# Optimization experiments

Measured on AMD Instinct MI355X. Metric: run time of the kernel, lower is better.

## Reference

```python
import jax, jax.numpy as jnp
import numpy as np

BN_EPS = 1e-5
N_NODES = 100000
N_EDGES = 1600000
IN_DIM = 128
HID = 256   # 2 * out_dim
OUT_DIM = 128


def setup_inputs() -> dict:
    key = jax.random.key(0)
    ks = jax.random.split(key, 8)
    x = jax.random.normal(ks[0], (N_NODES, IN_DIM), dtype=jnp.float32)
    edge_index = jax.random.randint(ks[1], (2, N_EDGES), 0, N_NODES, dtype=jnp.int32)
    # GINConv learned eps (train_eps=True), init 0
    eps = jnp.zeros((), dtype=jnp.float32)
    # MLP: Linear(in, 2*out) -> BN -> ReLU -> Linear(2*out, out)
    s1 = 1.0 / np.sqrt(IN_DIM)
    s2 = 1.0 / np.sqrt(HID)
    W1 = jax.random.uniform(ks[2], (IN_DIM, HID), jnp.float32, -s1, s1)
    b1 = jax.random.uniform(ks[3], (HID,), jnp.float32, -s1, s1)
    g1 = jnp.ones((HID,), jnp.float32)
    beta1 = jnp.zeros((HID,), jnp.float32)
    W2 = jax.random.uniform(ks[4], (HID, OUT_DIM), jnp.float32, -s2, s2)
    b2 = jax.random.uniform(ks[5], (OUT_DIM,), jnp.float32, -s2, s2)
    # outer BatchNorm
    g2 = jnp.ones((OUT_DIM,), jnp.float32)
    beta2 = jnp.zeros((OUT_DIM,), jnp.float32)
    return {"x": x, "edge_index": edge_index, "eps": eps,
            "W1": W1, "b1": b1, "g1": g1, "beta1": beta1,
            "W2": W2, "b2": b2, "g2": g2, "beta2": beta2}


def _batchnorm(h, gamma, beta):
    # training-mode BatchNorm1d: batch mean, biased variance
    mu = jnp.mean(h, axis=0)
    var = jnp.mean(jnp.square(h - mu), axis=0)
    return (h - mu) * jax.lax.rsqrt(var + BN_EPS) * gamma + beta


def reference(x, edge_index, eps, W1, b1, g1, beta1, W2, b2, g2, beta2):
    src, dst = edge_index[0], edge_index[1]
    # sum-aggregation of neighbor features: scatter-add x[src] onto dst
    aggr = jax.ops.segment_sum(x[src], dst, num_segments=x.shape[0])  # [N, in_dim]
    h = (1.0 + eps) * x + aggr
    # MLP: Linear -> BN -> ReLU -> Linear
    h = h @ W1 + b1
    h = jax.nn.relu(_batchnorm(h, g1, beta1))
    h = h @ W2 + b2
    # outer BN + ReLU
    return jax.nn.relu(_batchnorm(h, g2, beta2))
```

## Files before the change

### kernel.cpp

```cpp
#include <hip/hip_runtime.h>
#include <hip/hip_bf16.h>

#define N_NODES 100000
#define N_EDGES 1600000
#define IN_DIM  128
#define HID     256
#define OUT_DIM 128
#define BN_EPS  1e-5f

typedef unsigned int u32;
typedef unsigned short u16;
typedef __attribute__((ext_vector_type(8))) short short8v;
typedef __attribute__((ext_vector_type(4))) float f32x4;

__device__ __forceinline__ float bf2f(u16 h) {
    return __uint_as_float(((u32)h) << 16);
}
__device__ __forceinline__ u16 f2bf(float f) {
    u32 u = __float_as_uint(f);
    u32 r = (u + 0x7fffu + ((u >> 16) & 1u)) >> 16;
    return (u16)r;
}
__device__ __forceinline__ u32 pack2(float a, float b) {
    return (u32)f2bf(a) | ((u32)f2bf(b) << 16);
}
__device__ __forceinline__ void gload16(const void* g, void* l) {
    __builtin_amdgcn_global_load_lds((const __attribute__((address_space(1))) u32*)g,
                                     (__attribute__((address_space(3))) u32*)l, 16, 0, 0);
}
#define MFMA(a,b,c) __builtin_amdgcn_mfma_f32_16x16x32_bf16(a, b, c, 0, 0, 0)

__global__ __launch_bounds__(256) void k_prep(const float* __restrict__ x,
                                              const int* __restrict__ ei,
                                              const float* __restrict__ W1,
                                              const float* __restrict__ W2,
                                              uint2* __restrict__ xb,
                                              int* __restrict__ head2,
                                              int2* __restrict__ nxt,
                                              char* __restrict__ w1t,
                                              char* __restrict__ w2t) {
    int t = blockIdx.x * 256 + threadIdx.x;
    {
        float4 v = ((const float4*)x)[t];
        uint2 p;
        p.x = pack2(v.x, v.y);
        p.y = pack2(v.z, v.w);
        xb[t] = p;
    }
    if (t < N_EDGES) {
        int dst = ei[N_EDGES + t];
        int src = ei[t];
        int old = atomicExch(&head2[dst * 2 + (t & 1)], t);
        nxt[t] = make_int2(old, src);
    }
    if (t < 8192) {
        u16 tmp[8];
        if (t < 4096) {
            int j = t >> 4, kc = t & 15;
            #pragma unroll
            for (int i = 0; i < 8; ++i) tmp[i] = f2bf(W1[(kc * 8 + i) * HID + j]);
            u32 off = ((u32)(j * 256 + kc * 16)) ^ (((u32)(j & 7)) << 4);
            uint4 q;
            q.x = (u32)tmp[0] | ((u32)tmp[1] << 16);
            q.y = (u32)tmp[2] | ((u32)tmp[3] << 16);
            q.z = (u32)tmp[4] | ((u32)tmp[5] << 16);
            q.w = (u32)tmp[6] | ((u32)tmp[7] << 16);
            *(uint4*)(w1t + off) = q;
        } else {
            int t2 = t - 4096;
            int j = t2 >> 5, kc = t2 & 31;
            #pragma unroll
            for (int i = 0; i < 8; ++i) tmp[i] = f2bf(W2[(kc * 8 + i) * OUT_DIM + j]);
            u32 off = ((u32)(j * 512 + kc * 16)) ^ (((u32)(j & 7)) << 4);
            uint4 q;
            q.x = (u32)tmp[0] | ((u32)tmp[1] << 16);
            q.y = (u32)tmp[2] | ((u32)tmp[3] << 16);
            q.z = (u32)tmp[4] | ((u32)tmp[5] << 16);
            q.w = (u32)tmp[6] | ((u32)tmp[7] << 16);
            *(uint4*)(w2t + off) = q;
        }
    }
}

__global__ __launch_bounds__(256) void k_aggregate(const uint4* __restrict__ xb4,
                                                   const int2* __restrict__ nxt,
                                                   const int* __restrict__ head2,
                                                   const float* __restrict__ epsp,
                                                   char* __restrict__ aggrb) {
    const int lane = threadIdx.x & 63;
    const int w = threadIdx.x >> 6;
    const int q = lane >> 4, l = lane & 15;
    const int nq = q >> 1, p = q & 1;
    const int node = blockIdx.x * 8 + w * 2 + nq;

    float a[8];
    #pragma unroll
    for (int i = 0; i < 8; ++i) a[i] = 0.f;

    if (p == 0) {
        float sc = 1.0f + epsp[0];
        uint4 v = xb4[node * 16 + l];
        a[0] = bf2f((u16)v.x) * sc;  a[1] = bf2f((u16)(v.x >> 16)) * sc;
        a[2] = bf2f((u16)v.y) * sc;  a[3] = bf2f((u16)(v.y >> 16)) * sc;
        a[4] = bf2f((u16)v.z) * sc;  a[5] = bf2f((u16)(v.z >> 16)) * sc;
        a[6] = bf2f((u16)v.w) * sc;  a[7] = bf2f((u16)(v.w >> 16)) * sc;
    }
    int e = head2[node * 2 + p];
    while (e >= 0) {
        int2 nv = nxt[e];
        e = nv.x;
        uint4 v = xb4[nv.y * 16 + l];
        a[0] += bf2f((u16)v.x);  a[1] += bf2f((u16)(v.x >> 16));
        a[2] += bf2f((u16)v.y);  a[3] += bf2f((u16)(v.y >> 16));
        a[4] += bf2f((u16)v.z);  a[5] += bf2f((u16)(v.z >> 16));
        a[6] += bf2f((u16)v.w);  a[7] += bf2f((u16)(v.w >> 16));
    }
    #pragma unroll
    for (int i = 0; i < 8; ++i) a[i] += __shfl_xor(a[i], 16);
    if (p == 0) {
        uint4 o;
        o.x = pack2(a[0], a[1]);
        o.y = pack2(a[2], a[3]);
        o.z = pack2(a[4], a[5]);
        o.w = pack2(a[6], a[7]);
        u32 b = ((u32)node * 256 + (u32)l * 16) ^ (((u32)(node & 7)) << 4);
        *(uint4*)(aggrb + b) = o;
    }
}

__global__ __launch_bounds__(512) void k_gemm1(const char* __restrict__ aggrb,
                                               const char* __restrict__ w1t,
                                               const float* __restrict__ b1,
                                               u16* __restrict__ h1u,
                                               float* __restrict__ gstats) {
    __shared__ u16 Als[160 * 128];
    __shared__ u16 Bls[256 * 128];
    __shared__ float slds[512];

    const int tid = threadIdx.x, lane = tid & 63, w = tid >> 6;
    const int wr = w >> 2, wc = w & 3;
    const int base = blockIdx.x * 160;

    slds[tid] = 0.f;

    char* lA = (char*)Als;
    char* lB = (char*)Bls;
    const char* ga = aggrb + (size_t)base * 256;
    #pragma unroll
    for (int i = 0; i < 5; ++i)
        gload16(ga + i * 8192 + w * 1024 + (lane << 4), lA + i * 8192 + w * 1024);
    #pragma unroll
    for (int i = 0; i < 8; ++i)
        gload16(w1t + i * 8192 + w * 1024 + (lane << 4), lB + i * 8192 + w * 1024);

    const int rA = lane & 15;
    const int kb = (lane >> 4) << 3;
    const u32 xsw = ((u32)(rA & 7)) << 4;
    int colv[4]; float bcol[4];
    #pragma unroll
    for (int n = 0; n < 4; ++n) { colv[n] = wc * 64 + n * 16 + rA; bcol[n] = b1[colv[n]]; }

    asm volatile("s_waitcnt vmcnt(0)" ::: "memory");
    __syncthreads();

    f32x4 acc[5][4];
    #pragma unroll
    for (int m = 0; m < 5; ++m)
        #pragma unroll
        for (int n = 0; n < 4; ++n) acc[m][n] = (f32x4){0.f, 0.f, 0.f, 0.f};

    #pragma unroll
    for (int ks = 0; ks < 4; ++ks) {
        const int kk2 = (ks * 32 + kb) * 2;
        short8v a[5], b[4];
        #pragma unroll
        for (int m = 0; m < 5; ++m) {
            u32 off = ((u32)((wr * 80 + m * 16 + rA) * 256 + kk2)) ^ xsw;
            a[m] = *(const short8v*)(lA + off);
        }
        #pragma unroll
        for (int n = 0; n < 4; ++n) {
            u32 off = ((u32)(colv[n] * 256 + kk2)) ^ xsw;
            b[n] = *(const short8v*)(lB + off);
        }
        #pragma unroll
        for (int m = 0; m < 5; ++m)
            #pragma unroll
            for (int n = 0; n < 4; ++n)
                acc[m][n] = MFMA(a[m], b[n], acc[m][n]);
    }

    float csum[4] = {0.f,0.f,0.f,0.f}, csq[4] = {0.f,0.f,0.f,0.f};
    #pragma unroll
    for (int m = 0; m < 5; ++m) {
        int r0 = base + wr * 80 + m * 16 + ((lane >> 4) << 2);
        #pragma unroll
        for (int n = 0; n < 4; ++n) {
            f32x4 d = acc[m][n];
            #pragma unroll
            for (int r = 0; r < 4; ++r) {
                float v = d[r] + bcol[n];
                csum[n] += v; csq[n] += v * v;
                h1u[(size_t)(r0 + r) * 256 + colv[n]] = f2bf(v);
            }
        }
    }
    #pragma unroll
    for (int n = 0; n < 4; ++n) {
        csum[n] += __shfl_xor(csum[n], 16); csum[n] += __shfl_xor(csum[n], 32);
        csq[n]  += __shfl_xor(csq[n], 16);  csq[n]  += __shfl_xor(csq[n], 32);
    }
    if (lane < 16) {
        #pragma unroll
        for (int n = 0; n < 4; ++n) {
            atomicAdd(&slds[colv[n]], csum[n]);
            atomicAdd(&slds[256 + colv[n]], csq[n]);
        }
    }
    __syncthreads();
    atomicAdd(&gstats[tid], slds[tid]);
}

__global__ __launch_bounds__(512) void k_gemm2(const u16* __restrict__ h1u,
                                               const char* __restrict__ w2t,
                                               const float* __restrict__ b2,
                                               const float* __restrict__ g1,
                                               const float* __restrict__ beta1,
                                               const float* __restrict__ gstats,
                                               u16* __restrict__ h2b,
                                               float* __restrict__ gstats2) {
    __shared__ u16 Als[160 * 128];
    __shared__ u16 Bls[128 * 256];
    __shared__ float a1s[256], b1s[256];
    __shared__ float slds[256];

    const int tid = threadIdx.x, lane = tid & 63, w = tid >> 6;
    const int wr = w >> 2, wc = w & 3;
    const int base = blockIdx.x * 160;

    if (tid < 256) {
        float s = gstats[tid], sq = gstats[256 + tid];
        float mu = s * (1.0f / N_NODES);
        float var = sq * (1.0f / N_NODES) - mu * mu;
        float inv = rsqrtf(var + BN_EPS);
        float a = g1[tid] * inv;
        a1s[tid] = a;
        b1s[tid] = beta1[tid] - mu * a;
        slds[tid] = 0.f;
    }

    char* lA = (char*)Als;
    char* lB = (char*)Bls;
    #pragma unroll
    for (int i = 0; i < 8; ++i)
        gload16(w2t + i * 8192 + w * 1024 + (lane << 4), lB + i * 8192 + w * 1024);

    const int rA = lane & 15;
    const int kb = (lane >> 4) << 3;
    const u32 xsw = ((u32)(rA & 7)) << 4;
    int colv[2]; float bcol[2];
    #pragma unroll
    for (int n = 0; n < 2; ++n) { colv[n] = wc * 32 + n * 16 + rA; bcol[n] = b2[colv[n]]; }

    __syncthreads();

    f32x4 acc[5][2];
    #pragma unroll
    for (int m = 0; m < 5; ++m)
        #pragma unroll
        for (int n = 0; n < 2; ++n) acc[m][n] = (f32x4){0.f, 0.f, 0.f, 0.f};

    for (int kh = 0; kh < 2; ++kh) {
        #pragma unroll
        for (int i = 0; i < 10; ++i) {
            int id = tid + i * 512;
            int r = id >> 5;
            int c = id & 31;
            uint2 v = *(const uint2*)(h1u + (size_t)(base + r) * 256 + kh * 128 + c * 4);
            int cg = kh * 128 + c * 4;
            float4 av = *(const float4*)&a1s[cg];
            float4 bv = *(const float4*)&b1s[cg];
            float f0 = fmaxf(bf2f((u16)v.x)         * av.x + bv.x, 0.f);
            float f1 = fmaxf(bf2f((u16)(v.x >> 16)) * av.y + bv.y, 0.f);
            float f2 = fmaxf(bf2f((u16)v.y)         * av.z + bv.z, 0.f);
            float f3 = fmaxf(bf2f((u16)(v.y >> 16)) * av.w + bv.w, 0.f);
            uint2 p; p.x = pack2(f0, f1); p.y = pack2(f2, f3);
            u32 off = ((u32)(r * 256 + c * 8)) ^ (((u32)(r & 7)) << 4);
            *(uint2*)(lA + off) = p;
        }
        if (kh == 0) asm volatile("s_waitcnt vmcnt(0)" ::: "memory");
        __syncthreads();

        #pragma unroll
        for (int ks = 0; ks < 4; ++ks) {
            const int kk2 = (ks * 32 + kb) * 2;
            short8v a[5], b[2];
            #pragma unroll
            for (int m = 0; m < 5; ++m) {
                u32 off = ((u32)((wr * 80 + m * 16 + rA) * 256 + kk2)) ^ xsw;
                a[m] = *(const short8v*)(lA + off);
            }
            #pragma unroll
            for (int n = 0; n < 2; ++n) {
                u32 off = ((u32)(colv[n] * 512 + kh * 256 + kk2)) ^ xsw;
                b[n] = *(const short8v*)(lB + off);
            }
            #pragma unroll
            for (int m = 0; m < 5; ++m)
                #pragma unroll
                for (int n = 0; n < 2; ++n)
                    acc[m][n] = MFMA(a[m], b[n], acc[m][n]);
        }
        __syncthreads();
    }

    float csum[2] = {0.f,0.f}, csq[2] = {0.f,0.f};
    #pragma unroll
    for (int m = 0; m < 5; ++m) {
        int r0 = base + wr * 80 + m * 16 + ((lane >> 4) << 2);
        #pragma unroll
        for (int n = 0; n < 2; ++n) {
            f32x4 d = acc[m][n];
            #pragma unroll
            for (int r = 0; r < 4; ++r) {
                float v = d[r] + bcol[n];
                csum[n] += v; csq[n] += v * v;
                h2b[(size_t)(r0 + r) * 128 + colv[n]] = f2bf(v);
            }
        }
    }
    #pragma unroll
    for (int n = 0; n < 2; ++n) {
        csum[n] += __shfl_xor(csum[n], 16); csum[n] += __shfl_xor(csum[n], 32);
        csq[n]  += __shfl_xor(csq[n], 16);  csq[n]  += __shfl_xor(csq[n], 32);
    }
    if (lane < 16) {
        #pragma unroll
        for (int n = 0; n < 2; ++n) {
            atomicAdd(&slds[colv[n]], csum[n]);
            atomicAdd(&slds[128 + colv[n]], csq[n]);
        }
    }
    __syncthreads();
    if (tid < 256) atomicAdd(&gstats2[tid], slds[tid]);
}

__global__ __launch_bounds__(256) void k_bn2(const uint4* __restrict__ h2b4,
                                             float* __restrict__ out,
                                             const float* __restrict__ gstats2,
                                             const float* __restrict__ g2,
                                             const float* __restrict__ beta2) {
    int i = blockIdx.x * 256 + threadIdx.x;
    const int total = N_NODES * 16;
    if (i >= total) return;
    uint4 v = h2b4[i];
    int c0 = (i & 15) * 8;
    u16 hv[8] = {(u16)v.x, (u16)(v.x >> 16), (u16)v.y, (u16)(v.y >> 16),
                 (u16)v.z, (u16)(v.z >> 16), (u16)v.w, (u16)(v.w >> 16)};
    float res[8];
    #pragma unroll
    for (int j = 0; j < 8; ++j) {
        int c = c0 + j;
        float s = gstats2[c], sq = gstats2[OUT_DIM + c];
        float mu = s * (1.0f / N_NODES);
        float var = sq * (1.0f / N_NODES) - mu * mu;
        float inv = rsqrtf(var + BN_EPS);
        float a = g2[c] * inv;
        float b = beta2[c] - mu * a;
        res[j] = fmaxf(bf2f(hv[j]) * a + b, 0.f);
    }
    ((float4*)out)[i * 2]     = make_float4(res[0], res[1], res[2], res[3]);
    ((float4*)out)[i * 2 + 1] = make_float4(res[4], res[5], res[6], res[7]);
}

extern "C" void kernel_launch(void* const* d_in, const int* in_sizes, int n_in,
                              void* d_out, int out_size, void* d_ws, size_t ws_size,
                              hipStream_t stream) {
    const float* x     = (const float*)d_in[0];
    const int*   ei    = (const int*)d_in[1];
    const float* epsp  = (const float*)d_in[2];
    const float* W1    = (const float*)d_in[3];
    const float* b1    = (const float*)d_in[4];
    const float* g1    = (const float*)d_in[5];
    const float* beta1 = (const float*)d_in[6];
    const float* W2    = (const float*)d_in[7];
    const float* b2    = (const float*)d_in[8];
    const float* g2    = (const float*)d_in[9];
    const float* beta2 = (const float*)d_in[10];

    char* ws = (char*)d_ws;
    char*  aggrb   = ws;
    u16*   h2b     = (u16*)ws;
    u16*   h1u     = (u16*)(ws + 25600000);
    int2*  nxt     = (int2*)(ws + 25600000);
    int*   head2   = (int*)(ws + 38400000);
    uint2* xb      = (uint2*)(ws + 39200000);
    float* gstats  = (float*)(ws + 76800000);
    float* gstats2 = gstats + 512;
    char*  w1t     = ws + 76804096;
    char*  w2t     = ws + 76869632;
    float* out = (float*)d_out;

    hipMemsetAsync(head2, 0xFF, 800000, stream);
    hipMemsetAsync(gstats, 0, 768 * sizeof(float), stream);

    k_prep<<<12500, 256, 0, stream>>>(x, ei, W1, W2, xb, head2, nxt, w1t, w2t);
    k_aggregate<<<N_NODES / 8, 256, 0, stream>>>((const uint4*)xb, nxt, head2, epsp, aggrb);
    k_gemm1<<<625, 512, 0, stream>>>(aggrb, w1t, b1, h1u, gstats);
    k_gemm2<<<625, 512, 0, stream>>>(h1u, w2t, b2, g1, beta1, gstats, h2b, gstats2);
    k_bn2<<<(N_NODES * 16 + 255) / 256, 256, 0, stream>>>((const uint4*)h2b, out, gstats2, g2, beta2);
}
```

Measured before the change: 259.1 us.

## Read GEMM weight fragments directly from global memory instead of staging in LDS

Both GEMM kernels stop copying the transposed bf16 weight matrices into shared memory and instead load the B fragments straight from global (L2-resident) memory. The weight layout drops its XOR swizzle to match the direct reads. LDS use per block falls by 64 KB, and launch bounds now request more resident blocks, aiming at higher occupancy and less staging overhead. In exchange, each wave issues redundant global loads for the weights inside the MFMA loop, which adds latency that occupancy has to hide.

```diff
diff --git a/kernel.cpp b/kernel.cpp
--- a/kernel.cpp
+++ b/kernel.cpp
@@ -59,7 +59,7 @@
             int j = t >> 4, kc = t & 15;
             #pragma unroll
             for (int i = 0; i < 8; ++i) tmp[i] = f2bf(W1[(kc * 8 + i) * HID + j]);
-            u32 off = ((u32)(j * 256 + kc * 16)) ^ (((u32)(j & 7)) << 4);
+            u32 off = (u32)(j * 256 + kc * 16);
             uint4 q;
             q.x = (u32)tmp[0] | ((u32)tmp[1] << 16);
             q.y = (u32)tmp[2] | ((u32)tmp[3] << 16);
@@ -71,7 +71,7 @@
             int j = t2 >> 5, kc = t2 & 31;
             #pragma unroll
             for (int i = 0; i < 8; ++i) tmp[i] = f2bf(W2[(kc * 8 + i) * OUT_DIM + j]);
-            u32 off = ((u32)(j * 512 + kc * 16)) ^ (((u32)(j & 7)) << 4);
+            u32 off = (u32)(j * 512 + kc * 16);
             uint4 q;
             q.x = (u32)tmp[0] | ((u32)tmp[1] << 16);
             q.y = (u32)tmp[2] | ((u32)tmp[3] << 16);
@@ -128,13 +128,12 @@
     }
 }
 
-__global__ __launch_bounds__(512) void k_gemm1(const char* __restrict__ aggrb,
-                                               const char* __restrict__ w1t,
-                                               const float* __restrict__ b1,
-                                               u16* __restrict__ h1u,
-                                               float* __restrict__ gstats) {
+__global__ __launch_bounds__(512, 6) void k_gemm1(const char* __restrict__ aggrb,
+                                                  const char* __restrict__ w1t,
+                                                  const float* __restrict__ b1,
+                                                  u16* __restrict__ h1u,
+                                                  float* __restrict__ gstats) {
     __shared__ u16 Als[160 * 128];
-    __shared__ u16 Bls[256 * 128];
     __shared__ float slds[512];
 
     const int tid = threadIdx.x, lane = tid & 63, w = tid >> 6;
@@ -144,14 +143,10 @@
     slds[tid] = 0.f;
 
     char* lA = (char*)Als;
-    char* lB = (char*)Bls;
     const char* ga = aggrb + (size_t)base * 256;
     #pragma unroll
     for (int i = 0; i < 5; ++i)
         gload16(ga + i * 8192 + w * 1024 + (lane << 4), lA + i * 8192 + w * 1024);
-    #pragma unroll
-    for (int i = 0; i < 8; ++i)
-        gload16(w1t + i * 8192 + w * 1024 + (lane << 4), lB + i * 8192 + w * 1024);
 
     const int rA = lane & 15;
     const int kb = (lane >> 4) << 3;
@@ -174,14 +169,12 @@
         const int kk2 = (ks * 32 + kb) * 2;
         short8v a[5], b[4];
         #pragma unroll
+        for (int n = 0; n < 4; ++n)
+            b[n] = *(const short8v*)(w1t + colv[n] * 256 + kk2);
+        #pragma unroll
         for (int m = 0; m < 5; ++m) {
             u32 off = ((u32)((wr * 80 + m * 16 + rA) * 256 + kk2)) ^ xsw;
             a[m] = *(const short8v*)(lA + off);
-        }
-        #pragma unroll
-        for (int n = 0; n < 4; ++n) {
-            u32 off = ((u32)(colv[n] * 256 + kk2)) ^ xsw;
-            b[n] = *(const short8v*)(lB + off);
         }
         #pragma unroll
         for (int m = 0; m < 5; ++m)
@@ -221,16 +214,15 @@
     atomicAdd(&gstats[tid], slds[tid]);
 }
 
-__global__ __launch_bounds__(512) void k_gemm2(const u16* __restrict__ h1u,
-                                               const char* __restrict__ w2t,
-                                               const float* __restrict__ b2,
-                                               const float* __restrict__ g1,
-                                               const float* __restrict__ beta1,
-                                               const float* __restrict__ gstats,
-                                               u16* __restrict__ h2b,
-                                               float* __restrict__ gstats2) {
+__global__ __launch_bounds__(512, 6) void k_gemm2(const u16* __restrict__ h1u,
+                                                  const char* __restrict__ w2t,
+                                                  const float* __restrict__ b2,
+                                                  const float* __restrict__ g1,
+                                                  const float* __restrict__ beta1,
+                                                  const float* __restrict__ gstats,
+                                                  u16* __restrict__ h2b,
+                                                  float* __restrict__ gstats2) {
     __shared__ u16 Als[160 * 128];
-    __shared__ u16 Bls[128 * 256];
     __shared__ float a1s[256], b1s[256];
     __shared__ float slds[256];
 
@@ -250,10 +242,6 @@
     }
 
     char* lA = (char*)Als;
-    char* lB = (char*)Bls;
-    #pragma unroll
-    for (int i = 0; i < 8; ++i)
-        gload16(w2t + i * 8192 + w * 1024 + (lane << 4), lB + i * 8192 + w * 1024);
 
     const int rA = lane & 15;
     const int kb = (lane >> 4) << 3;
@@ -288,7 +276,6 @@
             u32 off = ((u32)(r * 256 + c * 8)) ^ (((u32)(r & 7)) << 4);
             *(uint2*)(lA + off) = p;
         }
-        if (kh == 0) asm volatile("s_waitcnt vmcnt(0)" ::: "memory");
         __syncthreads();
 
         #pragma unroll
@@ -296,14 +283,12 @@
             const int kk2 = (ks * 32 + kb) * 2;
             short8v a[5], b[2];
             #pragma unroll
+            for (int n = 0; n < 2; ++n)
+                b[n] = *(const short8v*)(w2t + colv[n] * 512 + kh * 256 + kk2);
+            #pragma unroll
             for (int m = 0; m < 5; ++m) {
                 u32 off = ((u32)((wr * 80 + m * 16 + rA) * 256 + kk2)) ^ xsw;
                 a[m] = *(const short8v*)(lA + off);
-            }
-            #pragma unroll
-            for (int n = 0; n < 2; ++n) {
-                u32 off = ((u32)(colv[n] * 512 + kh * 256 + kk2)) ^ xsw;
-                b[n] = *(const short8v*)(lB + off);
             }
             #pragma unroll
             for (int m = 0; m < 5; ++m)
```

Result: slower. 352.8 us (+36.2%).

## Store GEMM intermediates in MFMA-tile-native layout with vectorized epilogue writes

Applied to the files above, without the earlier changes.

Both GEMM epilogues now write their bf16 results in a tiled layout that follows the MFMA accumulator fragment: 16-row tiles, column-major within each tile. Each lane emits one 8-byte store instead of four scattered 2-byte stores. gemm2 and the final BN kernel read this layout back, transposing through LDS with scalar 2-byte LDS writes, and k_bn2 stages rows through shared memory so its fp32 output stores stay coalesced. The aim is to cut uncoalesced global stores in the epilogues, at the cost of more LDS traffic and possible bank conflicts in the consumers.

```diff
diff --git a/kernel.cpp b/kernel.cpp
--- a/kernel.cpp
+++ b/kernel.cpp
@@ -131,7 +131,7 @@
 __global__ __launch_bounds__(512) void k_gemm1(const char* __restrict__ aggrb,
                                                const char* __restrict__ w1t,
                                                const float* __restrict__ b1,
-                                               u16* __restrict__ h1u,
+                                               u16* __restrict__ h1t,
                                                float* __restrict__ gstats) {
     __shared__ u16 Als[160 * 128];
     __shared__ u16 Bls[256 * 128];
@@ -154,7 +154,8 @@
         gload16(w1t + i * 8192 + w * 1024 + (lane << 4), lB + i * 8192 + w * 1024);
 
     const int rA = lane & 15;
-    const int kb = (lane >> 4) << 3;
+    const int q = lane >> 4;
+    const int kb = q << 3;
     const u32 xsw = ((u32)(rA & 7)) << 4;
     int colv[4]; float bcol[4];
     #pragma unroll
@@ -190,19 +191,20 @@
                 acc[m][n] = MFMA(a[m], b[n], acc[m][n]);
     }
 
+    const int Tb = blockIdx.x * 10 + wr * 5;
     float csum[4] = {0.f,0.f,0.f,0.f}, csq[4] = {0.f,0.f,0.f,0.f};
     #pragma unroll
     for (int m = 0; m < 5; ++m) {
-        int r0 = base + wr * 80 + m * 16 + ((lane >> 4) << 2);
+        int T = Tb + m;
         #pragma unroll
         for (int n = 0; n < 4; ++n) {
             f32x4 d = acc[m][n];
-            #pragma unroll
-            for (int r = 0; r < 4; ++r) {
-                float v = d[r] + bcol[n];
-                csum[n] += v; csq[n] += v * v;
-                h1u[(size_t)(r0 + r) * 256 + colv[n]] = f2bf(v);
-            }
+            float v0 = d[0] + bcol[n], v1 = d[1] + bcol[n];
+            float v2 = d[2] + bcol[n], v3 = d[3] + bcol[n];
+            csum[n] += v0 + v1 + v2 + v3;
+            csq[n]  += v0*v0 + v1*v1 + v2*v2 + v3*v3;
+            uint2 p; p.x = pack2(v0, v1); p.y = pack2(v2, v3);
+            *(uint2*)(h1t + (size_t)T * 4096 + colv[n] * 16 + q * 4) = p;
         }
     }
     #pragma unroll
@@ -221,13 +223,13 @@
     atomicAdd(&gstats[tid], slds[tid]);
 }
 
-__global__ __launch_bounds__(512) void k_gemm2(const u16* __restrict__ h1u,
+__global__ __launch_bounds__(512) void k_gemm2(const uint4* __restrict__ h1t4,
                                                const char* __restrict__ w2t,
                                                const float* __restrict__ b2,
                                                const float* __restrict__ g1,
                                                const float* __restrict__ beta1,
                                                const float* __restrict__ gstats,
-                                               u16* __restrict__ h2b,
+                                               u16* __restrict__ h2t,
                                                float* __restrict__ gstats2) {
     __shared__ u16 Als[160 * 128];
     __shared__ u16 Bls[128 * 256];
@@ -236,7 +238,7 @@
 
     const int tid = threadIdx.x, lane = tid & 63, w = tid >> 6;
     const int wr = w >> 2, wc = w & 3;
-    const int base = blockIdx.x * 160;
+    const int Tbase = blockIdx.x * 10;
 
     if (tid < 256) {
         float s = gstats[tid], sq = gstats[256 + tid];
@@ -256,7 +258,8 @@
         gload16(w2t + i * 8192 + w * 1024 + (lane << 4), lB + i * 8192 + w * 1024);
 
     const int rA = lane & 15;
-    const int kb = (lane >> 4) << 3;
+    const int q = lane >> 4;
+    const int kb = q << 3;
     const u32 xsw = ((u32)(rA & 7)) << 4;
     int colv[2]; float bcol[2];
     #pragma unroll
@@ -272,21 +275,24 @@
 
     for (int kh = 0; kh < 2; ++kh) {
         #pragma unroll
-        for (int i = 0; i < 10; ++i) {
-            int id = tid + i * 512;
-            int r = id >> 5;
-            int c = id & 31;
-            uint2 v = *(const uint2*)(h1u + (size_t)(base + r) * 256 + kh * 128 + c * 4);
-            int cg = kh * 128 + c * 4;
-            float4 av = *(const float4*)&a1s[cg];
-            float4 bv = *(const float4*)&b1s[cg];
-            float f0 = fmaxf(bf2f((u16)v.x)         * av.x + bv.x, 0.f);
-            float f1 = fmaxf(bf2f((u16)(v.x >> 16)) * av.y + bv.y, 0.f);
-            float f2 = fmaxf(bf2f((u16)v.y)         * av.z + bv.z, 0.f);
-            float f3 = fmaxf(bf2f((u16)(v.y >> 16)) * av.w + bv.w, 0.f);
-            uint2 p; p.x = pack2(f0, f1); p.y = pack2(f2, f3);
-            u32 off = ((u32)(r * 256 + c * 8)) ^ (((u32)(r & 7)) << 4);
-            *(uint2*)(lA + off) = p;
+        for (int i = 0; i < 5; ++i) {
+            int id = i * 512 + tid;
+            int kl = id & 127;
+            int h16 = (id >> 7) & 1;
+            int Tl = id >> 8;
+            int kg = kh * 128 + kl;
+            uint4 v = h1t4[(size_t)(Tbase + Tl) * 512 + kg * 2 + h16];
+            float a = a1s[kg], b = b1s[kg];
+            int r0 = Tl * 16 + h16 * 8;
+            u16 hv[8] = {(u16)v.x, (u16)(v.x >> 16), (u16)v.y, (u16)(v.y >> 16),
+                         (u16)v.z, (u16)(v.z >> 16), (u16)v.w, (u16)(v.w >> 16)};
+            #pragma unroll
+            for (int rr = 0; rr < 8; ++rr) {
+                float f = fmaxf(bf2f(hv[rr]) * a + b, 0.f);
+                int r = r0 + rr;
+                u32 off = ((u32)(r * 256 + kl * 2)) ^ (((u32)(r & 7)) << 4);
+                *(u16*)(lA + off) = f2bf(f);
+            }
         }
         if (kh == 0) asm volatile("s_waitcnt vmcnt(0)" ::: "memory");
         __syncthreads();
@@ -295,17 +301,17 @@
         for (int ks = 0; ks < 4; ++ks) {
             const int kk2 = (ks * 32 + kb) * 2;
             short8v a[5], b[2];
+            #pragma unroll
+            for (int n = 0; n < 2; ++n) {
+                u32 off = ((u32)(colv[n] * 512 + kh * 256 + kk2)) ^ xsw;
+                b[n] = *(const short8v*)(lB + off);
+            }
             #pragma unroll
             for (int m = 0; m < 5; ++m) {
                 u32 off = ((u32)((wr * 80 + m * 16 + rA) * 256 + kk2)) ^ xsw;
                 a[m] = *(const short8v*)(lA + off);
             }
             #pragma unroll
-            for (int n = 0; n < 2; ++n) {
-                u32 off = ((u32)(colv[n] * 512 + kh * 256 + kk2)) ^ xsw;
-                b[n] = *(const short8v*)(lB + off);
-            }
-            #pragma unroll
             for (int m = 0; m < 5; ++m)
                 #pragma unroll
                 for (int n = 0; n < 2; ++n)
@@ -314,19 +320,20 @@
         __syncthreads();
     }
 
+    const int Tb = Tbase + wr * 5;
     float csum[2] = {0.f,0.f}, csq[2] = {0.f,0.f};
     #pragma unroll
     for (int m = 0; m < 5; ++m) {
-        int r0 = base + wr * 80 + m * 16 + ((lane >> 4) << 2);
+        int T = Tb + m;
         #pragma unroll
         for (int n = 0; n < 2; ++n) {
             f32x4 d = acc[m][n];
-            #pragma unroll
-            for (int r = 0; r < 4; ++r) {
-                float v = d[r] + bcol[n];
-                csum[n] += v; csq[n] += v * v;
-                h2b[(size_t)(r0 + r) * 128 + colv[n]] = f2bf(v);
-            }
+            float v0 = d[0] + bcol[n], v1 = d[1] + bcol[n];
+            float v2 = d[2] + bcol[n], v3 = d[3] + bcol[n];
+            csum[n] += v0 + v1 + v2 + v3;
+            csq[n]  += v0*v0 + v1*v1 + v2*v2 + v3*v3;
+            uint2 p; p.x = pack2(v0, v1); p.y = pack2(v2, v3);
+            *(uint2*)(h2t + (size_t)T * 2048 + colv[n] * 16 + q * 4) = p;
         }
     }
     #pragma unroll
@@ -345,32 +352,49 @@
     if (tid < 256) atomicAdd(&gstats2[tid], slds[tid]);
 }
 
-__global__ __launch_bounds__(256) void k_bn2(const uint4* __restrict__ h2b4,
+__global__ __launch_bounds__(256) void k_bn2(const uint4* __restrict__ h2t4,
                                              float* __restrict__ out,
                                              const float* __restrict__ gstats2,
                                              const float* __restrict__ g2,
                                              const float* __restrict__ beta2) {
-    int i = blockIdx.x * 256 + threadIdx.x;
-    const int total = N_NODES * 16;
-    if (i >= total) return;
-    uint4 v = h2b4[i];
-    int c0 = (i & 15) * 8;
-    u16 hv[8] = {(u16)v.x, (u16)(v.x >> 16), (u16)v.y, (u16)(v.y >> 16),
-                 (u16)v.z, (u16)(v.z >> 16), (u16)v.w, (u16)(v.w >> 16)};
-    float res[8];
-    #pragma unroll
-    for (int j = 0; j < 8; ++j) {
-        int c = c0 + j;
-        float s = gstats2[c], sq = gstats2[OUT_DIM + c];
+    __shared__ float fl[32 * 128];
+    __shared__ float a2s[128], b2s[128];
+    const int tid = threadIdx.x;
+    if (tid < 128) {
+        float s = gstats2[tid], sq = gstats2[128 + tid];
         float mu = s * (1.0f / N_NODES);
         float var = sq * (1.0f / N_NODES) - mu * mu;
         float inv = rsqrtf(var + BN_EPS);
-        float a = g2[c] * inv;
-        float b = beta2[c] - mu * a;
-        res[j] = fmaxf(bf2f(hv[j]) * a + b, 0.f);
-    }
-    ((float4*)out)[i * 2]     = make_float4(res[0], res[1], res[2], res[3]);
-    ((float4*)out)[i * 2 + 1] = make_float4(res[4], res[5], res[6], res[7]);
+        float a = g2[tid] * inv;
+        a2s[tid] = a;
+        b2s[tid] = beta2[tid] - mu * a;
+    }
+    __syncthreads();
+    const int Tbase = blockIdx.x * 2;
+    #pragma unroll
+    for (int i = 0; i < 2; ++i) {
+        int id = i * 256 + tid;
+        int kl = id & 127;
+        int h16 = (id >> 7) & 1;
+        int Tl = id >> 8;
+        uint4 v = h2t4[(size_t)(Tbase + Tl) * 256 + kl * 2 + h16];
+        float a = a2s[kl], b = b2s[kl];
+        int r0 = Tl * 16 + h16 * 8;
+        u16 hv[8] = {(u16)v.x, (u16)(v.x >> 16), (u16)v.y, (u16)(v.y >> 16),
+                     (u16)v.z, (u16)(v.z >> 16), (u16)v.w, (u16)(v.w >> 16)};
+        #pragma unroll
+        for (int rr = 0; rr < 8; ++rr)
+            fl[(r0 + rr) * 128 + kl] = fmaxf(bf2f(hv[rr]) * a + b, 0.f);
+    }
+    __syncthreads();
+    #pragma unroll
+    for (int i = 0; i < 4; ++i) {
+        int id = i * 256 + tid;
+        int row = id >> 5;
+        int ch = id & 31;
+        float4 vv = *(const float4*)&fl[row * 128 + ch * 4];
+        ((float4*)out)[(size_t)(blockIdx.x * 32 + row) * 32 + ch] = vv;
+    }
 }
 
 extern "C" void kernel_launch(void* const* d_in, const int* in_sizes, int n_in,
@@ -390,8 +414,8 @@
 
     char* ws = (char*)d_ws;
     char*  aggrb   = ws;
-    u16*   h2b     = (u16*)ws;
-    u16*   h1u     = (u16*)(ws + 25600000);
+    u16*   h2t     = (u16*)ws;
+    u16*   h1t     = (u16*)(ws + 25600000);
     int2*  nxt     = (int2*)(ws + 25600000);
     int*   head2   = (int*)(ws + 38400000);
     uint2* xb      = (uint2*)(ws + 39200000);
@@ -406,7 +430,7 @@
 
     k_prep<<<12500, 256, 0, stream>>>(x, ei, W1, W2, xb, head2, nxt, w1t, w2t);
     k_aggregate<<<N_NODES / 8, 256, 0, stream>>>((const uint4*)xb, nxt, head2, epsp, aggrb);
-    k_gemm1<<<625, 512, 0, stream>>>(aggrb, w1t, b1, h1u, gstats);
-    k_gemm2<<<625, 512, 0, stream>>>(h1u, w2t, b2, g1, beta1, gstats, h2b, gstats2);
-    k_bn2<<<(N_NODES * 16 + 255) / 256, 256, 0, stream>>>((const uint4*)h2b, out, gstats2, g2, beta2);
-}
+    k_gemm1<<<625, 512, 0, stream>>>(aggrb, w1t, b1, h1t, gstats);
+    k_gemm2<<<625, 512, 0, stream>>>((const uint4*)h1t, w2t, b2, g1, beta1, gstats, h2t, gstats2);
+    k_bn2<<<3125, 256, 0, stream>>>((const uint4*)h2t, out, gstats2, g2, beta2);
+}
```

Measured after the change: 257.0 us. Within noise of the previous version (-0.8%).
